# Optimization experiments

Hardware: AMD Instinct MI355X
Metric: run time of the kernel (lower is better)

Reference implementation:

```python
import jax, jax.numpy as jnp
import numpy as np
import math

LOCAL_RADIUS = 2
NEG_INF = -1e9


def _bilinear_gather_shared(feat, sample):
    """Bilinear sample with zeros padding, align_corners=True semantics.
    feat: [b, c, h, w]; sample: [n, k, 2] pixel coords (x, y), shared across batch.
    Returns [b, c, n, k].
    """
    b, c, h, w = feat.shape
    x, y = sample[..., 0], sample[..., 1]  # [n, k]
    x0 = jnp.floor(x); y0 = jnp.floor(y)
    x1 = x0 + 1.0;     y1 = y0 + 1.0
    feat_flat = feat.reshape(b, c, h * w)

    def corner(xi, yi, wgt):
        valid = (xi >= 0) & (xi < w) & (yi >= 0) & (yi < h)
        xi_c = jnp.clip(xi, 0, w - 1).astype(jnp.int32)
        yi_c = jnp.clip(yi, 0, h - 1).astype(jnp.int32)
        idx = yi_c * w + xi_c                       # [n, k]
        vals = feat_flat[:, :, idx]                 # [b, c, n, k]
        wv = jnp.where(valid, wgt, 0.0)             # zeros padding
        return vals * wv[None, None]

    out = (corner(x0, y0, (x1 - x) * (y1 - y))
           + corner(x1, y0, (x - x0) * (y1 - y))
           + corner(x0, y1, (x1 - x) * (y - y0))
           + corner(x1, y1, (x - x0) * (y - y0)))
    return out


def local_correlation_softmax(f0, f1, radius):
    b, c, h, w = f0.shape
    ygrid, xgrid = jnp.meshgrid(jnp.arange(h, dtype=f0.dtype),
                                jnp.arange(w, dtype=f0.dtype), indexing='ij')
    coords = jnp.stack([xgrid, ygrid], axis=-1).reshape(h * w, 2)  # [n, 2] (x, y)

    offs = jnp.arange(-radius, radius + 1, dtype=f0.dtype)
    dyy, dxx = jnp.meshgrid(offs, offs, indexing='ij')
    win = jnp.stack([dxx, dyy], axis=-1).reshape(-1, 2)            # [K, 2]

    sample = coords[:, None, :] + win[None, :, :]                  # [n, K, 2]
    valid = ((sample[..., 0] >= 0) & (sample[..., 0] < w)
             & (sample[..., 1] >= 0) & (sample[..., 1] < h))       # [n, K]

    win_feat = _bilinear_gather_shared(f1, sample)                 # [b, c, n, K]
    f0_flat = f0.reshape(b, c, h * w)
    corr = jnp.einsum('bcn,bcnk->bnk', f0_flat, win_feat) / (c ** 0.5)
    corr = jnp.where(valid[None], corr, NEG_INF)
    prob = jax.nn.softmax(corr, axis=-1)                           # [b, n, K]
    corresp = jnp.einsum('bnk,nkt->bnt', prob, sample)             # [b, n, 2]
    corresp = corresp.reshape(b, h, w, 2).transpose(0, 3, 1, 2)    # [b, 2, h, w]
    init = jnp.stack([xgrid, ygrid], axis=0)[None]                 # [1, 2, h, w]
    return corresp - init


def setup_inputs() -> dict:
    key = jax.random.key(0)
    k0, k1, k2 = jax.random.split(key, 3)
    shape = (2, 64, 128, 128)
    return {
        'feature0': jax.random.normal(k0, shape, dtype=jnp.float32),
        'feature1': jax.random.normal(k1, shape, dtype=jnp.float32),
        'feature2': jax.random.normal(k2, shape, dtype=jnp.float32),
    }


def reference(feature0, feature1, feature2):
    r = LOCAL_RADIUS
    v_0_2 = local_correlation_softmax(feature0, feature2, r)
    v_1_2 = local_correlation_softmax(feature1, feature2, r)
    v_2_0 = local_correlation_softmax(feature2, feature0, r)
    v_2_1 = local_correlation_softmax(feature2, feature1, r)
    return jnp.stack([v_0_2, v_1_2, v_2_0, v_2_1], axis=0)  # [4, b, 2, h, w]
```

## Files before the change

### kernel.cpp

```cpp
#include <hip/hip_runtime.h>

#define H 128
#define W 128
#define C 64
#define HW (H * W)
#define RAD 2
#define KD 5
#define KK 25

#define TSX 16
#define TSY 8
#define HX 20
#define HY 12
#define RSTR 20
#define PLANE 244
#define CB 16
#define ROUNDS 4
#define LDSF (CB * PLANE)

__device__ inline float cs_reduce(float x)
{
    float a = x, b = x;
    asm("v_permlane16_swap_b32 %0, %1" : "+v"(a), "+v"(b));
    float s = a + b;
    float c = s, d = s;
    asm("v_permlane32_swap_b32 %0, %1" : "+v"(c), "+v"(d));
    return c + d;
}

__global__ __launch_bounds__(256, 4)
void bam_corr_softmax_kernel(const float* __restrict__ f0,
                             const float* __restrict__ f1,
                             const float* __restrict__ f2,
                             float* __restrict__ out)
{
    __shared__ float lds[LDSF];

    const int tid  = threadIdx.x;
    const int lane = tid & 63;
    const int wav  = tid >> 6;
    const int cs   = lane >> 4;
    const int s    = lane & 15;
    const int sy   = s >> 2;
    const int sxp  = s & 3;
    const int wx   = wav & 1;
    const int wy   = wav >> 1;
    const int lx   = wx * 8 + sxp * 2;
    const int ly   = wy * 4 + sy;

    const int i    = blockIdx.x;
    const int band = i & 7;
    const int j    = i >> 3;
    const int img  = j & 7;
    const int t    = j >> 3;
    const int tileX = t & 7;
    const int tileY = band * 2 + (t >> 3);

    const int v = img >> 1;
    const int b = img & 1;

    const float* A;
    const float* Bf;
    if (v == 0)      { A = f0; Bf = f2; }
    else if (v == 1) { A = f1; Bf = f2; }
    else if (v == 2) { A = f2; Bf = f0; }
    else             { A = f2; Bf = f1; }

    const int x0 = tileX * TSX;
    const int y0 = tileY * TSY;
    const int x  = x0 + lx;
    const int y  = y0 + ly;

    const float* Abase = A + (size_t)b * C * HW + (size_t)y * W + x;
    const float* Bbase = Bf + (size_t)b * C * HW;

    float c0[KK], c1[KK];
#pragma unroll
    for (int k = 0; k < KK; ++k) { c0[k] = 0.f; c1[k] = 0.f; }

    for (int r = 0; r < ROUNDS; ++r) {
#pragma unroll
        for (int it = 0; it < 4; ++it) {
            int q = tid + it * 256;
            if (q < CB * HY * 5) {
                int p   = q / 60;
                int rem = q - p * 60;
                int row = rem / 5;
                int c4  = rem - row * 5;
                int ch  = r * CB + p;
                int gy  = y0 - RAD + row;
                int gx  = x0 - RAD + c4 * 4;
                float4 val;
                if (gy >= 0 && gy < H && gx >= 0 && gx + 3 < W) {
                    val = *reinterpret_cast<const float4*>(
                        Bbase + (size_t)ch * HW + gy * W + gx);
                } else {
                    float vv[4];
#pragma unroll
                    for (int e = 0; e < 4; ++e) {
                        int gxe = gx + e;
                        vv[e] = (gy >= 0 && gy < H && gxe >= 0 && gxe < W)
                              ? Bbase[(size_t)ch * HW + (size_t)gy * W + gxe]
                              : 0.f;
                    }
                    val = make_float4(vv[0], vv[1], vv[2], vv[3]);
                }
                *reinterpret_cast<float4*>(&lds[p * PLANE + row * RSTR + c4 * 4]) = val;
            }
        }
        __syncthreads();

#pragma unroll
        for (int c = 0; c < 4; ++c) {
            const int pl = cs * 4 + c;
            const int ch = r * CB + pl;
            float2 a2 = *reinterpret_cast<const float2*>(Abase + (size_t)ch * HW);
            const float* bp = &lds[pl * PLANE + ly * RSTR + lx];
#pragma unroll
            for (int ky = 0; ky < KD; ++ky) {
                const float* rp = bp + ky * RSTR;
                float2 w01 = *reinterpret_cast<const float2*>(rp);
                float2 w23 = *reinterpret_cast<const float2*>(rp + 2);
                float2 w45 = *reinterpret_cast<const float2*>(rp + 4);
                const int kb = ky * KD;
                c0[kb + 0] = fmaf(a2.x, w01.x, c0[kb + 0]);
                c0[kb + 1] = fmaf(a2.x, w01.y, c0[kb + 1]);
                c0[kb + 2] = fmaf(a2.x, w23.x, c0[kb + 2]);
                c0[kb + 3] = fmaf(a2.x, w23.y, c0[kb + 3]);
                c0[kb + 4] = fmaf(a2.x, w45.x, c0[kb + 4]);
                c1[kb + 0] = fmaf(a2.y, w01.y, c1[kb + 0]);
                c1[kb + 1] = fmaf(a2.y, w23.x, c1[kb + 1]);
                c1[kb + 2] = fmaf(a2.y, w23.y, c1[kb + 2]);
                c1[kb + 3] = fmaf(a2.y, w45.x, c1[kb + 3]);
                c1[kb + 4] = fmaf(a2.y, w45.y, c1[kb + 4]);
            }
        }
        __syncthreads();
    }

#pragma unroll
    for (int k = 0; k < KK; ++k) {
        c0[k] = cs_reduce(c0[k]);
        c1[k] = cs_reduce(c1[k]);
    }

    const float scale = 0.125f;
    float ox0, oy0, ox1, oy1;
    {
        float m = -1e30f;
#pragma unroll
        for (int ky = 0; ky < KD; ++ky) {
            int syy = y + ky - RAD;
#pragma unroll
            for (int kx = 0; kx < KD; ++kx) {
                int sxx = x + kx - RAD;
                int k = ky * KD + kx;
                float cv = c0[k] * scale;
                bool valid = (sxx >= 0) && (sxx < W) && (syy >= 0) && (syy < H);
                cv = valid ? cv : -1e9f;
                c0[k] = cv;
                m = fmaxf(m, cv);
            }
        }
        float sum = 0.f, ox = 0.f, oy = 0.f;
#pragma unroll
        for (int ky = 0; ky < KD; ++ky)
#pragma unroll
            for (int kx = 0; kx < KD; ++kx) {
                int k = ky * KD + kx;
                float e = __expf(c0[k] - m);
                sum += e;
                ox += e * (float)(kx - RAD);
                oy += e * (float)(ky - RAD);
            }
        float inv = 1.f / sum;
        ox0 = ox * inv; oy0 = oy * inv;
    }
    {
        const int x1c = x + 1;
        float m = -1e30f;
#pragma unroll
        for (int ky = 0; ky < KD; ++ky) {
            int syy = y + ky - RAD;
#pragma unroll
            for (int kx = 0; kx < KD; ++kx) {
                int sxx = x1c + kx - RAD;
                int k = ky * KD + kx;
                float cv = c1[k] * scale;
                bool valid = (sxx >= 0) && (sxx < W) && (syy >= 0) && (syy < H);
                cv = valid ? cv : -1e9f;
                c1[k] = cv;
                m = fmaxf(m, cv);
            }
        }
        float sum = 0.f, ox = 0.f, oy = 0.f;
#pragma unroll
        for (int ky = 0; ky < KD; ++ky)
#pragma unroll
            for (int kx = 0; kx < KD; ++kx) {
                int k = ky * KD + kx;
                float e = __expf(c1[k] - m);
                sum += e;
                ox += e * (float)(kx - RAD);
                oy += e * (float)(ky - RAD);
            }
        float inv = 1.f / sum;
        ox1 = ox * inv; oy1 = oy * inv;
    }

    if (cs == 0) {
        size_t ob = ((size_t)img * 2) * HW + (size_t)y * W + x;
        *reinterpret_cast<float2*>(&out[ob])      = make_float2(ox0, ox1);
        *reinterpret_cast<float2*>(&out[ob + HW]) = make_float2(oy0, oy1);
    }
}

extern "C" void kernel_launch(void* const* d_in, const int* in_sizes, int n_in,
                              void* d_out, int out_size, void* d_ws, size_t ws_size,
                              hipStream_t stream)
{
    const float* f0 = (const float*)d_in[0];
    const float* f1 = (const float*)d_in[1];
    const float* f2 = (const float*)d_in[2];
    float* out = (float*)d_out;

    dim3 block(256, 1, 1);
    dim3 grid(1024, 1, 1);
    bam_corr_softmax_kernel<<<grid, block, 0, stream>>>(f0, f1, f2, out);
}
```

Baseline: 28.50 us.

## Compute 2x2 pixel blocks per thread with 16x16 tiles and 32-channel rounds

Each thread now computes a 2x2 pixel quad instead of a 1x2 pair, so six LDS rows are loaded per channel and reused across two output rows. The tile grows to 16x16 with a 32-channel LDS stage in two rounds, and the grid is halved. LDS reads per output and halo redundancy go down. In exchange, register pressure doubles (100 accumulators), which is why the launch bound drops to 2 blocks per SM, and there are fewer blocks to spread across CUs.

```diff
diff --git a/kernel.cpp b/kernel.cpp
--- a/kernel.cpp
+++ b/kernel.cpp
@@ -9,16 +9,17 @@
 #define KK 25
 
 #define TSX 16
-#define TSY 8
-#define HX 20
-#define HY 12
-#define RSTR 20
-#define PLANE 244
-#define CB 16
-#define ROUNDS 4
-#define LDSF (CB * PLANE)
-
-__device__ inline float cs_reduce(float x)
+#define TSY 16
+#define HROWS 20
+#define HCOLS 24
+#define RSTR 24
+#define PSTR 484
+#define GS   (8 * PSTR + 8)
+#define CB 32
+#define ROUNDS 2
+#define LDSF (4 * GS)
+
+__device__ __forceinline__ float cs_reduce(float x)
 {
     float a = x, b = x;
     asm("v_permlane16_swap_b32 %0, %1" : "+v"(a), "+v"(b));
@@ -28,7 +29,40 @@
     return c + d;
 }
 
-__global__ __launch_bounds__(256, 4)
+__device__ __forceinline__ float2 softmax_eo(float (&cr)[KK], int xx, int yy)
+{
+    const float scale = 0.125f;
+    float m = -1e30f;
+#pragma unroll
+    for (int ky = 0; ky < KD; ++ky) {
+        int syy = yy + ky - RAD;
+#pragma unroll
+        for (int kx = 0; kx < KD; ++kx) {
+            int sxx = xx + kx - RAD;
+            int k = ky * KD + kx;
+            float cv = cr[k] * scale;
+            bool valid = (sxx >= 0) && (sxx < W) && (syy >= 0) && (syy < H);
+            cv = valid ? cv : -1e9f;
+            cr[k] = cv;
+            m = fmaxf(m, cv);
+        }
+    }
+    float sum = 0.f, ox = 0.f, oy = 0.f;
+#pragma unroll
+    for (int ky = 0; ky < KD; ++ky)
+#pragma unroll
+        for (int kx = 0; kx < KD; ++kx) {
+            int k = ky * KD + kx;
+            float e = __expf(cr[k] - m);
+            sum += e;
+            ox += e * (float)(kx - RAD);
+            oy += e * (float)(ky - RAD);
+        }
+    float inv = 1.f / sum;
+    return make_float2(ox * inv, oy * inv);
+}
+
+__global__ __launch_bounds__(256, 2)
 void bam_corr_softmax_kernel(const float* __restrict__ f0,
                              const float* __restrict__ f1,
                              const float* __restrict__ f2,
@@ -41,20 +75,16 @@
     const int wav  = tid >> 6;
     const int cs   = lane >> 4;
     const int s    = lane & 15;
-    const int sy   = s >> 2;
-    const int sxp  = s & 3;
-    const int wx   = wav & 1;
-    const int wy   = wav >> 1;
-    const int lx   = wx * 8 + sxp * 2;
-    const int ly   = wy * 4 + sy;
-
-    const int i    = blockIdx.x;
-    const int band = i & 7;
-    const int j    = i >> 3;
-    const int img  = j & 7;
-    const int t    = j >> 3;
-    const int tileX = t & 7;
-    const int tileY = band * 2 + (t >> 3);
+    const int qx   = s & 7;
+    const int qy   = wav * 2 + (s >> 3);
+    const int lx   = qx * 2;
+    const int ly   = qy * 2;
+
+    const int i     = blockIdx.x;
+    const int band  = i & 7;
+    const int j     = i >> 3;
+    const int img   = j & 7;
+    const int tileX = j >> 3;
 
     const int v = img >> 1;
     const int b = img & 1;
@@ -67,72 +97,73 @@
     else             { A = f2; Bf = f1; }
 
     const int x0 = tileX * TSX;
-    const int y0 = tileY * TSY;
+    const int y0 = band * TSY;
     const int x  = x0 + lx;
     const int y  = y0 + ly;
 
-    const float* Abase = A + (size_t)b * C * HW + (size_t)y * W + x;
+    const float* Arow  = A + (size_t)b * C * HW + (size_t)y * W + x;
     const float* Bbase = Bf + (size_t)b * C * HW;
 
-    float c0[KK], c1[KK];
-#pragma unroll
-    for (int k = 0; k < KK; ++k) { c0[k] = 0.f; c1[k] = 0.f; }
-
-    for (int r = 0; r < ROUNDS; ++r) {
-#pragma unroll
-        for (int it = 0; it < 4; ++it) {
-            int q = tid + it * 256;
-            if (q < CB * HY * 5) {
-                int p   = q / 60;
-                int rem = q - p * 60;
-                int row = rem / 5;
-                int c4  = rem - row * 5;
-                int ch  = r * CB + p;
-                int gy  = y0 - RAD + row;
-                int gx  = x0 - RAD + c4 * 4;
-                float4 val;
-                if (gy >= 0 && gy < H && gx >= 0 && gx + 3 < W) {
-                    val = *reinterpret_cast<const float4*>(
-                        Bbase + (size_t)ch * HW + gy * W + gx);
-                } else {
-                    float vv[4];
-#pragma unroll
-                    for (int e = 0; e < 4; ++e) {
-                        int gxe = gx + e;
-                        vv[e] = (gy >= 0 && gy < H && gxe >= 0 && gxe < W)
-                              ? Bbase[(size_t)ch * HW + (size_t)gy * W + gxe]
-                              : 0.f;
-                    }
-                    val = make_float4(vv[0], vv[1], vv[2], vv[3]);
+    float c00[KK], c01[KK], c10[KK], c11[KK];
+#pragma unroll
+    for (int k = 0; k < KK; ++k) { c00[k]=0.f; c01[k]=0.f; c10[k]=0.f; c11[k]=0.f; }
+
+    for (int rnd = 0; rnd < ROUNDS; ++rnd) {
+        for (int q = tid; q < CB * HROWS * 6; q += 256) {
+            int p   = q / (HROWS * 6);
+            int rem = q - p * (HROWS * 6);
+            int row = rem / 6;
+            int c6  = rem - row * 6;
+            int ch  = rnd * CB + p;
+            int gy  = y0 - 2 + row;
+            int gx  = x0 - 4 + c6 * 4;
+            float4 val;
+            if (gy >= 0 && gy < H && gx >= 0 && gx + 3 < W) {
+                val = *reinterpret_cast<const float4*>(
+                    Bbase + (size_t)ch * HW + (size_t)(gy * W + gx));
+            } else {
+                float vv[4];
+#pragma unroll
+                for (int e = 0; e < 4; ++e) {
+                    int gxe = gx + e;
+                    vv[e] = (gy >= 0 && gy < H && gxe >= 0 && gxe < W)
+                          ? Bbase[(size_t)ch * HW + (size_t)(gy * W + gxe)]
+                          : 0.f;
                 }
-                *reinterpret_cast<float4*>(&lds[p * PLANE + row * RSTR + c4 * 4]) = val;
+                val = make_float4(vv[0], vv[1], vv[2], vv[3]);
             }
+            int g = p >> 3, c = p & 7;
+            *reinterpret_cast<float4*>(&lds[g * GS + c * PSTR + row * RSTR + c6 * 4]) = val;
         }
         __syncthreads();
 
 #pragma unroll
-        for (int c = 0; c < 4; ++c) {
-            const int pl = cs * 4 + c;
-            const int ch = r * CB + pl;
-            float2 a2 = *reinterpret_cast<const float2*>(Abase + (size_t)ch * HW);
-            const float* bp = &lds[pl * PLANE + ly * RSTR + lx];
-#pragma unroll
-            for (int ky = 0; ky < KD; ++ky) {
-                const float* rp = bp + ky * RSTR;
+        for (int c = 0; c < 8; ++c) {
+            const int ch = rnd * CB + cs * 8 + c;
+            float2 aT = *reinterpret_cast<const float2*>(Arow + (size_t)ch * HW);
+            float2 aB = *reinterpret_cast<const float2*>(Arow + (size_t)ch * HW + W);
+            const float* bp = &lds[cs * GS + c * PSTR + ly * RSTR + lx + 2];
+#pragma unroll
+            for (int rr = 0; rr < 6; ++rr) {
+                const float* rp = bp + rr * RSTR;
                 float2 w01 = *reinterpret_cast<const float2*>(rp);
                 float2 w23 = *reinterpret_cast<const float2*>(rp + 2);
                 float2 w45 = *reinterpret_cast<const float2*>(rp + 4);
-                const int kb = ky * KD;
-                c0[kb + 0] = fmaf(a2.x, w01.x, c0[kb + 0]);
-                c0[kb + 1] = fmaf(a2.x, w01.y, c0[kb + 1]);
-                c0[kb + 2] = fmaf(a2.x, w23.x, c0[kb + 2]);
-                c0[kb + 3] = fmaf(a2.x, w23.y, c0[kb + 3]);
-                c0[kb + 4] = fmaf(a2.x, w45.x, c0[kb + 4]);
-                c1[kb + 0] = fmaf(a2.y, w01.y, c1[kb + 0]);
-                c1[kb + 1] = fmaf(a2.y, w23.x, c1[kb + 1]);
-                c1[kb + 2] = fmaf(a2.y, w23.y, c1[kb + 2]);
-                c1[kb + 3] = fmaf(a2.y, w45.x, c1[kb + 3]);
-                c1[kb + 4] = fmaf(a2.y, w45.y, c1[kb + 4]);
+                float w[6] = { w01.x, w01.y, w23.x, w23.y, w45.x, w45.y };
+                if (rr < 5) {
+#pragma unroll
+                    for (int kx = 0; kx < KD; ++kx) {
+                        c00[rr*KD+kx] = fmaf(aT.x, w[kx],   c00[rr*KD+kx]);
+                        c01[rr*KD+kx] = fmaf(aT.y, w[kx+1], c01[rr*KD+kx]);
+                    }
+                }
+                if (rr >= 1) {
+#pragma unroll
+                    for (int kx = 0; kx < KD; ++kx) {
+                        c10[(rr-1)*KD+kx] = fmaf(aB.x, w[kx],   c10[(rr-1)*KD+kx]);
+                        c11[(rr-1)*KD+kx] = fmaf(aB.y, w[kx+1], c11[(rr-1)*KD+kx]);
+                    }
+                }
             }
         }
         __syncthreads();
@@ -140,78 +171,23 @@
 
 #pragma unroll
     for (int k = 0; k < KK; ++k) {
-        c0[k] = cs_reduce(c0[k]);
-        c1[k] = cs_reduce(c1[k]);
-    }
-
-    const float scale = 0.125f;
-    float ox0, oy0, ox1, oy1;
-    {
-        float m = -1e30f;
-#pragma unroll
-        for (int ky = 0; ky < KD; ++ky) {
-            int syy = y + ky - RAD;
-#pragma unroll
-            for (int kx = 0; kx < KD; ++kx) {
-                int sxx = x + kx - RAD;
-                int k = ky * KD + kx;
-                float cv = c0[k] * scale;
-                bool valid = (sxx >= 0) && (sxx < W) && (syy >= 0) && (syy < H);
-                cv = valid ? cv : -1e9f;
-                c0[k] = cv;
-                m = fmaxf(m, cv);
-            }
-        }
-        float sum = 0.f, ox = 0.f, oy = 0.f;
-#pragma unroll
-        for (int ky = 0; ky < KD; ++ky)
-#pragma unroll
-            for (int kx = 0; kx < KD; ++kx) {
-                int k = ky * KD + kx;
-                float e = __expf(c0[k] - m);
-                sum += e;
-                ox += e * (float)(kx - RAD);
-                oy += e * (float)(ky - RAD);
-            }
-        float inv = 1.f / sum;
-        ox0 = ox * inv; oy0 = oy * inv;
-    }
-    {
-        const int x1c = x + 1;
-        float m = -1e30f;
-#pragma unroll
-        for (int ky = 0; ky < KD; ++ky) {
-            int syy = y + ky - RAD;
-#pragma unroll
-            for (int kx = 0; kx < KD; ++kx) {
-                int sxx = x1c + kx - RAD;
-                int k = ky * KD + kx;
-                float cv = c1[k] * scale;
-                bool valid = (sxx >= 0) && (sxx < W) && (syy >= 0) && (syy < H);
-                cv = valid ? cv : -1e9f;
-                c1[k] = cv;
-                m = fmaxf(m, cv);
-            }
-        }
-        float sum = 0.f, ox = 0.f, oy = 0.f;
-#pragma unroll
-        for (int ky = 0; ky < KD; ++ky)
-#pragma unroll
-            for (int kx = 0; kx < KD; ++kx) {
-                int k = ky * KD + kx;
-                float e = __expf(c1[k] - m);
-                sum += e;
-                ox += e * (float)(kx - RAD);
-                oy += e * (float)(ky - RAD);
-            }
-        float inv = 1.f / sum;
-        ox1 = ox * inv; oy1 = oy * inv;
-    }
+        c00[k] = cs_reduce(c00[k]);
+        c01[k] = cs_reduce(c01[k]);
+        c10[k] = cs_reduce(c10[k]);
+        c11[k] = cs_reduce(c11[k]);
+    }
+
+    float2 r00 = softmax_eo(c00, x,     y);
+    float2 r01 = softmax_eo(c01, x + 1, y);
+    float2 r10 = softmax_eo(c10, x,     y + 1);
+    float2 r11 = softmax_eo(c11, x + 1, y + 1);
 
     if (cs == 0) {
         size_t ob = ((size_t)img * 2) * HW + (size_t)y * W + x;
-        *reinterpret_cast<float2*>(&out[ob])      = make_float2(ox0, ox1);
-        *reinterpret_cast<float2*>(&out[ob + HW]) = make_float2(oy0, oy1);
+        *reinterpret_cast<float2*>(&out[ob])          = make_float2(r00.x, r01.x);
+        *reinterpret_cast<float2*>(&out[ob + W])      = make_float2(r10.x, r11.x);
+        *reinterpret_cast<float2*>(&out[ob + HW])     = make_float2(r00.y, r01.y);
+        *reinterpret_cast<float2*>(&out[ob + HW + W]) = make_float2(r10.y, r11.y);
     }
 }
 
@@ -225,6 +201,6 @@
     float* out = (float*)d_out;
 
     dim3 block(256, 1, 1);
-    dim3 grid(1024, 1, 1);
+    dim3 grid(512, 1, 1);
     bam_corr_softmax_kernel<<<grid, block, 0, stream>>>(f0, f1, f2, out);
 }
```

After: 33.07 us. 16.0% more time.
